# Optimization experiments

Measured on AMD Instinct MI355X. Metric: run time of the kernel, lower is better.

Reference implementation:

```python
import jax, jax.numpy as jnp
import numpy as np

B, N, D, H = 8, 2048, 256, 8
HD = D // H  # head_dim = 32
LN_EPS = 1e-5


def setup_inputs() -> dict:
    key = jax.random.key(0)
    ks = jax.random.split(key, 8)
    x = jax.random.normal(ks[0], (B, N, D), dtype=jnp.float32)
    # dense 0/1 adjacency with guaranteed self-loops (avoids all -inf softmax rows)
    adj = jax.random.randint(ks[1], (B, N, N), 0, 2, dtype=jnp.int32)
    adj = jnp.maximum(adj, jnp.eye(N, dtype=jnp.int32)[None, :, :])
    s = 0.02
    Wq = jax.random.normal(ks[2], (D, D), dtype=jnp.float32) * s
    Wk = jax.random.normal(ks[3], (D, D), dtype=jnp.float32) * s
    Wv = jax.random.normal(ks[4], (D, D), dtype=jnp.float32) * s
    Wo = jax.random.normal(ks[5], (D, D), dtype=jnp.float32) * s
    zeros = jnp.zeros((D,), dtype=jnp.float32)
    return {
        "x": x, "adjacency": adj,
        "Wq": Wq, "bq": zeros, "Wk": Wk, "bk": zeros,
        "Wv": Wv, "bv": zeros, "Wo": Wo, "bo": zeros,
        "gamma": jnp.ones((D,), dtype=jnp.float32), "beta": zeros,
    }


def reference(x, adjacency, Wq, bq, Wk, bk, Wv, bv, Wo, bo, gamma, beta):
    b, n, d = x.shape
    q = (x @ Wq + bq).reshape(b, n, H, HD)
    k = (x @ Wk + bk).reshape(b, n, H, HD)
    v = (x @ Wv + bv).reshape(b, n, H, HD)
    # scores: [B, N(query), M(key), H]
    scores = jnp.einsum('bnhd,bmhd->bnmh', q, k) / jnp.sqrt(jnp.float32(HD))
    mask = (adjacency == 0)[..., None]  # [B,N,M,1] broadcasts over heads
    scores = jnp.where(mask, -jnp.inf, scores)
    weights = jax.nn.softmax(scores, axis=2)  # softmax over key axis m
    # dropout is identity in eval mode
    attended = jnp.einsum('bnmh,bmhd->bnhd', weights, v).reshape(b, n, d)
    out = attended @ Wo + bo
    out = out + x  # residual (output.shape == x.shape since input_dim == output_dim)
    mu = jnp.mean(out, axis=-1, keepdims=True)
    var = jnp.mean(jnp.square(out - mu), axis=-1, keepdims=True)
    return (out - mu) * jax.lax.rsqrt(var + LN_EPS) * gamma + beta
```

## Files before the change

### kernel.cpp

```cpp
#include <hip/hip_runtime.h>
#include <hip/hip_bf16.h>
#include <cstdint>
#include <cstddef>

#define B_ 8
#define N_ 2048
#define D_ 256
#define H_ 8
#define HD_ 32
#define LN_EPS 1e-5f
#define QSCALE 0.25506275f

typedef __attribute__((ext_vector_type(8))) short short8;
typedef __attribute__((ext_vector_type(4))) float f32x4;
typedef __attribute__((ext_vector_type(16))) float f32x16;

static __device__ __forceinline__ float exp2v(float x) {
#if __has_builtin(__builtin_amdgcn_exp2f)
    return __builtin_amdgcn_exp2f(x);
#else
    float r;
    asm("v_exp_f32 %0, %1" : "=v"(r) : "v"(x));
    return r;
#endif
}

static __device__ __forceinline__ unsigned short f2bf(float f) {
    union { float f; unsigned int u; } v; v.f = f;
    unsigned int r = v.u + 0x7fffu + ((v.u >> 16) & 1u);
    return (unsigned short)(r >> 16);
}

static __device__ __forceinline__ unsigned int cvtpk(float lo, float hi) {
    unsigned int d;
    asm("v_cvt_pk_bf16_f32 %0, %1, %2" : "=v"(d) : "v"(lo), "v"(hi));
    return d;
}

__global__ __launch_bounds__(256) void k_prep_w(const float* __restrict__ w0, const float* __restrict__ w1,
                                                const float* __restrict__ w2, const float* __restrict__ w3,
                                                unsigned short* __restrict__ wt) {
    int c = blockIdx.x, mat = blockIdx.y, k = threadIdx.x;
    const float* w = (mat == 0) ? w0 : (mat == 1) ? w1 : (mat == 2) ? w2 : w3;
    wt[((size_t)(mat * 256 + c)) * 256 + k] = f2bf(w[k * 256 + c]);
}

__global__ __launch_bounds__(256) void k_mask(const int* __restrict__ adj,
                                              unsigned int* __restrict__ mbg) {
    int wave = (blockIdx.x * 256 + threadIdx.x) >> 6;
    int lane = threadIdx.x & 63;
    const int* p = adj + (size_t)wave * 1024 + lane;
    unsigned long long* outp = reinterpret_cast<unsigned long long*>(mbg) + (size_t)wave * 16;

    int v[16];
#pragma unroll
    for (int i = 0; i < 16; ++i)
        v[i] = p[i * 64];
    __builtin_amdgcn_sched_barrier(0);

#pragma unroll
    for (int i = 0; i < 16; ++i) {
        unsigned long long m = __ballot(v[i] != 0);
        if (lane == 0) outp[i] = m;
    }
}

__global__ __launch_bounds__(256) void k_maskT2(const unsigned int* __restrict__ mbg,
                                                unsigned int* __restrict__ mbgT2) {
    __shared__ unsigned int bits[64][65];
    int tid = threadIdx.x, lane = tid & 63, wv = tid >> 6;
    int b = blockIdx.x >> 5, qg = blockIdx.x & 31;

    {
        int row = tid >> 2, cc = (tid & 3) * 16;
        const uint4* src = reinterpret_cast<const uint4*>(
            mbg + ((size_t)(b * N_ + qg * 64 + row)) * 64 + cc);
#pragma unroll
        for (int j = 0; j < 4; ++j) {
            uint4 v = src[j];
            bits[row][cc + 4 * j + 0] = v.x; bits[row][cc + 4 * j + 1] = v.y;
            bits[row][cc + 4 * j + 2] = v.z; bits[row][cc + 4 * j + 3] = v.w;
        }
    }
    __syncthreads();

    int h = lane >> 5, l31 = lane & 31;
    const unsigned int M[5] = {0x0000FFFFu, 0x00FF00FFu, 0x0F0F0F0Fu, 0x33333333u, 0x55555555u};
#pragma unroll
    for (int j = 0; j < 16; ++j) {
        int kw = wv * 16 + j;
        unsigned int w = bits[lane][kw];
#pragma unroll
        for (int si = 0; si < 5; ++si) {
            int s = 16 >> si;
            unsigned int m = M[si];
            unsigned int t = (unsigned int)__shfl_xor((int)w, s, 64);
            unsigned int a = (w & m) | ((t & m) << s);
            unsigned int c = (w & ~m) | ((t >> s) & m);
            w = (lane & s) ? c : a;
        }
        int k = kw * 32 + l31;
        int kp = (k & ~7) | ((k & 3) << 1) | ((k >> 2) & 1);
        mbgT2[((size_t)(b * 64 + qg * 2 + h)) * 2048 + kp] = w;
    }
}

__global__ __launch_bounds__(256) void k_qkv(const float* __restrict__ x,
                                             const unsigned short* __restrict__ wt,
                                             const float* __restrict__ bq, const float* __restrict__ bk,
                                             const float* __restrict__ bv,
                                             unsigned short* __restrict__ Qb, unsigned short* __restrict__ Kb,
                                             unsigned short* __restrict__ Vs) {
    int mat = blockIdx.y;
    int lane = threadIdx.x & 63;
    int wv = threadIdx.x >> 6;
    int row0 = blockIdx.x * 64 + wv * 16;
    int l15 = lane & 15, lg = lane >> 4;
    const float* bias = (mat == 0) ? bq : (mat == 1) ? bk : bv;
    const float qs = (mat == 0) ? QSCALE : 1.0f;
    const unsigned short* wm = wt + (size_t)mat * 65536;

    short8 af[8];
    const float* xrow = x + (size_t)(row0 + l15) * 256 + lg * 8;
#pragma unroll
    for (int kk = 0; kk < 8; ++kk) {
        float4 a = *reinterpret_cast<const float4*>(xrow + kk * 32);
        float4 b = *reinterpret_cast<const float4*>(xrow + kk * 32 + 4);
        union { short8 s8; unsigned int u[4]; } t;
        t.u[0] = cvtpk(a.x, a.y); t.u[1] = cvtpk(a.z, a.w);
        t.u[2] = cvtpk(b.x, b.y); t.u[3] = cvtpk(b.z, b.w);
        af[kk] = t.s8;
    }

    int b = row0 >> 11;
    int nbase = (row0 & 2047) + lg * 4;

    for (int ci = 0; ci < 16; ++ci) {
        const unsigned short* wrow = wm + (size_t)(ci * 16 + l15) * 256 + lg * 8;
        f32x4 acc = {0.f, 0.f, 0.f, 0.f};
#pragma unroll
        for (int kk = 0; kk < 8; ++kk) {
            short8 bfg = *reinterpret_cast<const short8*>(wrow + kk * 32);
            acc = __builtin_amdgcn_mfma_f32_16x16x32_bf16(af[kk], bfg, acc, 0, 0, 0);
        }
        int col = ci * 16 + l15;
        float bcol = bias[col];
        int h = col >> 5, hd = col & 31;
        if (mat < 2) {
            unsigned short* dst = (mat == 0) ? Qb : Kb;
#pragma unroll
            for (int r = 0; r < 4; ++r) {
                size_t off = ((size_t)(b * 8 + h) * 2048 + nbase + r) * 32 + hd;
                dst[off] = f2bf((acc[r] + bcol) * qs);
            }
        } else {
            size_t off = (size_t)(b * 8 + h) * 65536
                       + ((size_t)(nbase >> 4) * 32 + hd) * 16 + (nbase & 15);
            ushort4 o;
            o.x = f2bf(acc[0] + bcol); o.y = f2bf(acc[1] + bcol);
            o.z = f2bf(acc[2] + bcol); o.w = f2bf(acc[3] + bcol);
            *reinterpret_cast<ushort4*>(Vs + off) = o;
        }
    }
}

#define SL(j, offs) asm("s_load_dwordx2 %0, %1, " offs : "=s"(m##j) : "s"(mbase))
#define SLOAD16() do { \
    SL(0, "0x0");  SL(1, "0x8");  SL(2, "0x10"); SL(3, "0x18"); \
    SL(4, "0x20"); SL(5, "0x28"); SL(6, "0x30"); SL(7, "0x38"); \
    SL(8, "0x40"); SL(9, "0x48"); SL(10, "0x50"); SL(11, "0x58"); \
    SL(12, "0x60"); SL(13, "0x68"); SL(14, "0x70"); SL(15, "0x78"); } while (0)
#define CND(d, s_, mj) asm("v_cndmask_b32 %0, 0, %1, %2" : "=v"(d) : "v"(s_), "s"(mj))

__global__ __launch_bounds__(256, 5) void k_attn(const unsigned short* __restrict__ Qb,
                                                 const unsigned short* __restrict__ Kb,
                                                 const unsigned short* __restrict__ Vs,
                                                 const unsigned int* __restrict__ mbgT2,
                                                 unsigned short* __restrict__ att) {
    int tid = threadIdx.x;
    int lane = tid & 63;
    int l31 = lane & 31, hi = lane >> 5;
    int b = blockIdx.x & 7;
    int hg = (blockIdx.x >> 3) & 1;
    int qt32 = blockIdx.x >> 4;
    int q0 = qt32 * 32;
    int head = hg * 4 + (tid >> 6);
    int bh = b * 8 + head;

    const unsigned short* Qh = Qb + (size_t)bh * N_ * HD_;
    const unsigned short* Kh = Kb + (size_t)bh * N_ * HD_;
    const unsigned short* Vh = Vs + (size_t)bh * 65536;

    short8 qf0 = *reinterpret_cast<const short8*>(Qh + (size_t)(q0 + l31) * HD_ + hi * 8);
    short8 qf1 = *reinterpret_cast<const short8*>(Qh + (size_t)(q0 + l31) * HD_ + hi * 8 + 16);
    const unsigned short* krow = Kh + (size_t)l31 * HD_ + hi * 8;
    const unsigned short* vfp = Vh + (size_t)l31 * 16 + hi * 8;

    unsigned long long mbase = (unsigned long long)(mbgT2 + (size_t)(b * 64 + qt32) * 2048);
    unsigned long long m0, m1, m2, m3, m4, m5, m6, m7, m8, m9, m10, m11, m12, m13, m14, m15;
    SLOAD16();

    const f32x16 fz = {0.f,0.f,0.f,0.f,0.f,0.f,0.f,0.f,0.f,0.f,0.f,0.f,0.f,0.f,0.f,0.f};
    f32x16 attacc = fz;
    float lsum = 0.f;

#pragma unroll 1
    for (int t = 0; t < 64; ++t) {
        short8 kf0 = *reinterpret_cast<const short8*>(krow + (size_t)t * 1024);
        short8 kf1 = *reinterpret_cast<const short8*>(krow + (size_t)t * 1024 + 16);
        short8 vf0 = *reinterpret_cast<const short8*>(vfp + (size_t)t * 1024);
        short8 vf1 = *reinterpret_cast<const short8*>(vfp + (size_t)t * 1024 + 512);

        __builtin_amdgcn_s_setprio(1);
        f32x16 s = __builtin_amdgcn_mfma_f32_32x32x16_bf16(kf0, qf0, fz, 0, 0, 0);
        s = __builtin_amdgcn_mfma_f32_32x32x16_bf16(kf1, qf1, s, 0, 0, 0);
        __builtin_amdgcn_s_setprio(0);

        float e0 = exp2v(s[0]),  e1 = exp2v(s[1]),  e2 = exp2v(s[2]),  e3 = exp2v(s[3]);
        float e4 = exp2v(s[4]),  e5 = exp2v(s[5]),  e6 = exp2v(s[6]),  e7 = exp2v(s[7]);
        float e8 = exp2v(s[8]),  e9 = exp2v(s[9]),  e10 = exp2v(s[10]), e11 = exp2v(s[11]);
        float e12 = exp2v(s[12]), e13 = exp2v(s[13]), e14 = exp2v(s[14]), e15 = exp2v(s[15]);

        asm volatile("s_waitcnt lgkmcnt(0)"
                     : "+s"(m0), "+s"(m1), "+s"(m2), "+s"(m3), "+s"(m4), "+s"(m5), "+s"(m6), "+s"(m7),
                       "+s"(m8), "+s"(m9), "+s"(m10), "+s"(m11), "+s"(m12), "+s"(m13), "+s"(m14), "+s"(m15));

        float p0, p1, p2, p3, p4, p5, p6, p7, p8, p9, p10, p11, p12, p13, p14, p15;
        CND(p0, e0, m0);   CND(p1, e1, m1);   CND(p2, e2, m2);   CND(p3, e3, m3);
        CND(p4, e4, m4);   CND(p5, e5, m5);   CND(p6, e6, m6);   CND(p7, e7, m7);
        CND(p8, e8, m8);   CND(p9, e9, m9);   CND(p10, e10, m10); CND(p11, e11, m11);
        CND(p12, e12, m12); CND(p13, e13, m13); CND(p14, e14, m14); CND(p15, e15, m15);

        lsum += ((p0 + p1) + (p2 + p3)) + ((p4 + p5) + (p6 + p7))
              + ((p8 + p9) + (p10 + p11)) + ((p12 + p13) + (p14 + p15));

        unsigned int pd[4][2];
        pd[0][0] = cvtpk(p0, p1);   pd[0][1] = cvtpk(p2, p3);
        pd[1][0] = cvtpk(p4, p5);   pd[1][1] = cvtpk(p6, p7);
        pd[2][0] = cvtpk(p8, p9);   pd[2][1] = cvtpk(p10, p11);
        pd[3][0] = cvtpk(p12, p13); pd[3][1] = cvtpk(p14, p15);

        mbase += 128;
        SLOAD16();

        asm("v_permlane32_swap_b32 %0, %1" : "+v"(pd[0][0]), "+v"(pd[1][0]));
        asm("v_permlane32_swap_b32 %0, %1" : "+v"(pd[0][1]), "+v"(pd[1][1]));
        asm("v_permlane32_swap_b32 %0, %1" : "+v"(pd[2][0]), "+v"(pd[3][0]));
        asm("v_permlane32_swap_b32 %0, %1" : "+v"(pd[2][1]), "+v"(pd[3][1]));

        union { short8 s8; unsigned int u[4]; } bf0, bf1;
        bf0.u[0] = pd[0][0]; bf0.u[1] = pd[0][1]; bf0.u[2] = pd[1][0]; bf0.u[3] = pd[1][1];
        bf1.u[0] = pd[2][0]; bf1.u[1] = pd[2][1]; bf1.u[2] = pd[3][0]; bf1.u[3] = pd[3][1];

        __builtin_amdgcn_s_setprio(1);
        attacc = __builtin_amdgcn_mfma_f32_32x32x16_bf16(vf0, bf0.s8, attacc, 0, 0, 0);
        attacc = __builtin_amdgcn_mfma_f32_32x32x16_bf16(vf1, bf1.s8, attacc, 0, 0, 0);
        __builtin_amdgcn_s_setprio(0);
    }

    lsum += __shfl_xor(lsum, 32, 64);
    float rcp = 1.f / lsum;

    unsigned short* arow = att + ((size_t)b * N_ + q0 + l31) * D_ + head * HD_;
#pragma unroll
    for (int g = 0; g < 4; ++g) {
        ushort4 o;
        o.x = f2bf(attacc[4 * g + 0] * rcp);
        o.y = f2bf(attacc[4 * g + 1] * rcp);
        o.z = f2bf(attacc[4 * g + 2] * rcp);
        o.w = f2bf(attacc[4 * g + 3] * rcp);
        *reinterpret_cast<ushort4*>(arow + 8 * g + 4 * hi) = o;
    }
}

__global__ __launch_bounds__(256) void k_outln(const unsigned short* __restrict__ att,
                                               const unsigned short* __restrict__ wot,
                                               const float* __restrict__ bo,
                                               const float* __restrict__ x,
                                               const float* __restrict__ gamma, const float* __restrict__ beta,
                                               float* __restrict__ out) {
    int lane = threadIdx.x & 63, wv = threadIdx.x >> 6;
    int l15 = lane & 15, lg = lane >> 4;
    int row0 = blockIdx.x * 64 + wv * 16;

    short8 af[8];
    const unsigned short* arow = att + (size_t)(row0 + l15) * 256 + lg * 8;
#pragma unroll
    for (int kk = 0; kk < 8; ++kk)
        af[kk] = *reinterpret_cast<const short8*>(arow + kk * 32);

    float v[16][4];
#pragma unroll
    for (int ci = 0; ci < 16; ++ci) {
        const unsigned short* wrow = wot + (size_t)(ci * 16 + l15) * 256 + lg * 8;
        f32x4 acc = {0.f, 0.f, 0.f, 0.f};
#pragma unroll
        for (int kk = 0; kk < 8; ++kk) {
            short8 bfg = *reinterpret_cast<const short8*>(wrow + kk * 32);
            acc = __builtin_amdgcn_mfma_f32_16x16x32_bf16(af[kk], bfg, acc, 0, 0, 0);
        }
        float bcol = bo[ci * 16 + l15];
#pragma unroll
        for (int r = 0; r < 4; ++r)
            v[ci][r] = acc[r] + bcol + x[(size_t)(row0 + lg * 4 + r) * 256 + ci * 16 + l15];
    }

    float sum[4] = {0.f, 0.f, 0.f, 0.f}, sq[4] = {0.f, 0.f, 0.f, 0.f};
#pragma unroll
    for (int ci = 0; ci < 16; ++ci)
#pragma unroll
        for (int r = 0; r < 4; ++r) {
            sum[r] += v[ci][r];
            sq[r] += v[ci][r] * v[ci][r];
        }
#pragma unroll
    for (int d = 1; d < 16; d <<= 1)
#pragma unroll
        for (int r = 0; r < 4; ++r) {
            sum[r] += __shfl_xor(sum[r], d, 64);
            sq[r] += __shfl_xor(sq[r], d, 64);
        }

    float mu[4], rs[4];
#pragma unroll
    for (int r = 0; r < 4; ++r) {
        mu[r] = sum[r] * (1.f / 256.f);
        float var = sq[r] * (1.f / 256.f) - mu[r] * mu[r];
        rs[r] = rsqrtf(var + LN_EPS);
    }

#pragma unroll
    for (int ci = 0; ci < 16; ++ci) {
        float g = gamma[ci * 16 + l15], be = beta[ci * 16 + l15];
#pragma unroll
        for (int r = 0; r < 4; ++r)
            out[(size_t)(row0 + lg * 4 + r) * 256 + ci * 16 + l15] = (v[ci][r] - mu[r]) * rs[r] * g + be;
    }
}

extern "C" void kernel_launch(void* const* d_in, const int* in_sizes, int n_in,
                              void* d_out, int out_size, void* d_ws, size_t ws_size,
                              hipStream_t stream) {
    (void)in_sizes; (void)n_in; (void)out_size; (void)ws_size;
    const float* x     = (const float*)d_in[0];
    const int*   adj   = (const int*)d_in[1];
    const float* Wq    = (const float*)d_in[2];
    const float* bq    = (const float*)d_in[3];
    const float* Wk    = (const float*)d_in[4];
    const float* bk    = (const float*)d_in[5];
    const float* Wv    = (const float*)d_in[6];
    const float* bv    = (const float*)d_in[7];
    const float* Wo    = (const float*)d_in[8];
    const float* bo    = (const float*)d_in[9];
    const float* gamma = (const float*)d_in[10];
    const float* beta  = (const float*)d_in[11];
    float* out = (float*)d_out;

    char* ws = (char*)d_ws;
    unsigned short* wt   = (unsigned short*)ws; ws += (size_t)4 * 256 * 256 * 2;
    unsigned short* Qb   = (unsigned short*)ws; ws += (size_t)B_ * H_ * N_ * HD_ * 2;
    unsigned short* Kb   = (unsigned short*)ws; ws += (size_t)B_ * H_ * N_ * HD_ * 2;
    unsigned short* Vs   = (unsigned short*)ws; ws += (size_t)B_ * H_ * N_ * HD_ * 2;
    unsigned short* att  = (unsigned short*)ws; ws += (size_t)16384 * 256 * 2;
    unsigned int*   mbg  = (unsigned int*)ws;   ws += (size_t)B_ * N_ * 64 * 4;
    unsigned int*   mbgT2 = (unsigned int*)ws;  ws += (size_t)B_ * 64 * 2048 * 4 + 8192;

    k_prep_w<<<dim3(256, 4), 256, 0, stream>>>(Wq, Wk, Wv, Wo, wt);
    k_mask<<<8192, 256, 0, stream>>>(adj, mbg);
    k_maskT2<<<256, 256, 0, stream>>>(mbg, mbgT2);
    k_qkv<<<dim3(256, 3), 256, 0, stream>>>(x, wt, bq, bk, bv, Qb, Kb, Vs);
    k_attn<<<1024, 256, 0, stream>>>(Qb, Kb, Vs, mbgT2, att);
    k_outln<<<256, 256, 0, stream>>>(att, wt + 3 * 65536, bo, x, gamma, beta, out);
}
```

Measured before the change: 188.5 us.

## Fuse adjacency bit-packing with transpose and unroll attention loop without setprio

```diff
diff --git a/kernel.cpp b/kernel.cpp
--- a/kernel.cpp
+++ b/kernel.cpp
@@ -45,41 +45,29 @@
     wt[((size_t)(mat * 256 + c)) * 256 + k] = f2bf(w[k * 256 + c]);
 }
 
-__global__ __launch_bounds__(256) void k_mask(const int* __restrict__ adj,
-                                              unsigned int* __restrict__ mbg) {
-    int wave = (blockIdx.x * 256 + threadIdx.x) >> 6;
-    int lane = threadIdx.x & 63;
-    const int* p = adj + (size_t)wave * 1024 + lane;
-    unsigned long long* outp = reinterpret_cast<unsigned long long*>(mbg) + (size_t)wave * 16;
-
-    int v[16];
-#pragma unroll
-    for (int i = 0; i < 16; ++i)
-        v[i] = p[i * 64];
-    __builtin_amdgcn_sched_barrier(0);
-
-#pragma unroll
+__global__ __launch_bounds__(256) void k_maskF(const int* __restrict__ adj,
+                                               unsigned int* __restrict__ mbgT2) {
+    __shared__ unsigned int bits[64][66];
+    int tid = threadIdx.x, lane = tid & 63, wv = tid >> 6;
+    int b = blockIdx.x >> 5, rg = blockIdx.x & 31;
+
+    const int* base = adj + ((size_t)(b * N_ + rg * 64 + wv * 16)) * N_ + lane;
+#pragma unroll 1
     for (int i = 0; i < 16; ++i) {
-        unsigned long long m = __ballot(v[i] != 0);
-        if (lane == 0) outp[i] = m;
-    }
-}
-
-__global__ __launch_bounds__(256) void k_maskT2(const unsigned int* __restrict__ mbg,
-                                                unsigned int* __restrict__ mbgT2) {
-    __shared__ unsigned int bits[64][65];
-    int tid = threadIdx.x, lane = tid & 63, wv = tid >> 6;
-    int b = blockIdx.x >> 5, qg = blockIdx.x & 31;
-
-    {
-        int row = tid >> 2, cc = (tid & 3) * 16;
-        const uint4* src = reinterpret_cast<const uint4*>(
-            mbg + ((size_t)(b * N_ + qg * 64 + row)) * 64 + cc);
-#pragma unroll
-        for (int j = 0; j < 4; ++j) {
-            uint4 v = src[j];
-            bits[row][cc + 4 * j + 0] = v.x; bits[row][cc + 4 * j + 1] = v.y;
-            bits[row][cc + 4 * j + 2] = v.z; bits[row][cc + 4 * j + 3] = v.w;
+        const int* prow = base + (size_t)i * N_;
+#pragma unroll
+        for (int half = 0; half < 2; ++half) {
+            int v[16];
+#pragma unroll
+            for (int j = 0; j < 16; ++j)
+                v[j] = prow[half * 1024 + j * 64];
+            __builtin_amdgcn_sched_barrier(0);
+#pragma unroll
+            for (int j = 0; j < 16; ++j) {
+                unsigned long long m = __ballot(v[j] != 0);
+                if (lane == 0)
+                    *reinterpret_cast<unsigned long long*>(&bits[wv * 16 + i][half * 32 + 2 * j]) = m;
+            }
         }
     }
     __syncthreads();
@@ -101,7 +89,7 @@
         }
         int k = kw * 32 + l31;
         int kp = (k & ~7) | ((k & 3) << 1) | ((k >> 2) & 1);
-        mbgT2[((size_t)(b * 64 + qg * 2 + h)) * 2048 + kp] = w;
+        mbgT2[((size_t)(b * 64 + rg * 2 + h)) * 2048 + kp] = w;
     }
 }
 
@@ -204,17 +192,15 @@
     f32x16 attacc = fz;
     float lsum = 0.f;
 
-#pragma unroll 1
+#pragma unroll 2
     for (int t = 0; t < 64; ++t) {
         short8 kf0 = *reinterpret_cast<const short8*>(krow + (size_t)t * 1024);
         short8 kf1 = *reinterpret_cast<const short8*>(krow + (size_t)t * 1024 + 16);
         short8 vf0 = *reinterpret_cast<const short8*>(vfp + (size_t)t * 1024);
         short8 vf1 = *reinterpret_cast<const short8*>(vfp + (size_t)t * 1024 + 512);
 
-        __builtin_amdgcn_s_setprio(1);
         f32x16 s = __builtin_amdgcn_mfma_f32_32x32x16_bf16(kf0, qf0, fz, 0, 0, 0);
         s = __builtin_amdgcn_mfma_f32_32x32x16_bf16(kf1, qf1, s, 0, 0, 0);
-        __builtin_amdgcn_s_setprio(0);
 
         float e0 = exp2v(s[0]),  e1 = exp2v(s[1]),  e2 = exp2v(s[2]),  e3 = exp2v(s[3]);
         float e4 = exp2v(s[4]),  e5 = exp2v(s[5]),  e6 = exp2v(s[6]),  e7 = exp2v(s[7]);
@@ -252,10 +238,8 @@
         bf0.u[0] = pd[0][0]; bf0.u[1] = pd[0][1]; bf0.u[2] = pd[1][0]; bf0.u[3] = pd[1][1];
         bf1.u[0] = pd[2][0]; bf1.u[1] = pd[2][1]; bf1.u[2] = pd[3][0]; bf1.u[3] = pd[3][1];
 
-        __builtin_amdgcn_s_setprio(1);
         attacc = __builtin_amdgcn_mfma_f32_32x32x16_bf16(vf0, bf0.s8, attacc, 0, 0, 0);
         attacc = __builtin_amdgcn_mfma_f32_32x32x16_bf16(vf1, bf1.s8, attacc, 0, 0, 0);
-        __builtin_amdgcn_s_setprio(0);
     }
 
     lsum += __shfl_xor(lsum, 32, 64);
@@ -362,12 +346,10 @@
     unsigned short* Kb   = (unsigned short*)ws; ws += (size_t)B_ * H_ * N_ * HD_ * 2;
     unsigned short* Vs   = (unsigned short*)ws; ws += (size_t)B_ * H_ * N_ * HD_ * 2;
     unsigned short* att  = (unsigned short*)ws; ws += (size_t)16384 * 256 * 2;
-    unsigned int*   mbg  = (unsigned int*)ws;   ws += (size_t)B_ * N_ * 64 * 4;
     unsigned int*   mbgT2 = (unsigned int*)ws;  ws += (size_t)B_ * 64 * 2048 * 4 + 8192;
 
     k_prep_w<<<dim3(256, 4), 256, 0, stream>>>(Wq, Wk, Wv, Wo, wt);
-    k_mask<<<8192, 256, 0, stream>>>(adj, mbg);
-    k_maskT2<<<256, 256, 0, stream>>>(mbg, mbgT2);
+    k_maskF<<<256, 256, 0, stream>>>(adj, mbgT2);
     k_qkv<<<dim3(256, 3), 256, 0, stream>>>(x, wt, bq, bk, bv, Qb, Kb, Vs);
     k_attn<<<1024, 256, 0, stream>>>(Qb, Kb, Vs, mbgT2, att);
     k_outln<<<256, 256, 0, stream>>>(att, wt + 3 * 65536, bo, x, gamma, beta, out);
```

Result: no change. 187.8 us (-0.4%).
